# Optimization experiments

Hardware: AMD Instinct MI355X
Metric: run time of the kernel (lower is better)

Reference implementation:

```python
import jax, jax.numpy as jnp
import numpy as np

D = 1024
H = 4 * D
E = 8
K = 2


def setup_inputs() -> dict:
    key = jax.random.key(0)
    ks = jax.random.split(key, 8)
    s = 1.0 / np.sqrt(D)
    sh = 1.0 / np.sqrt(H)
    return {
        "x": jax.random.normal(ks[0], (4, 2048, D), dtype=jnp.float32),
        "gate_w": jax.random.uniform(ks[1], (D, E), jnp.float32, -s, s),
        "gate_b": jax.random.uniform(ks[2], (E,), jnp.float32, -s, s),
        "w1": jax.random.uniform(ks[3], (E, D, H), jnp.float32, -s, s),
        "b1": jax.random.uniform(ks[4], (E, H), jnp.float32, -s, s),
        "w2": jax.random.uniform(ks[5], (E, H, D), jnp.float32, -sh, sh),
        "b2": jax.random.uniform(ks[6], (E, D), jnp.float32, -sh, sh),
    }


def reference(x, gate_w, gate_b, w1, b1, w2, b2):
    # Gating: softmax over experts, top-k, renormalize.
    gate_logits = jnp.einsum("bsd,de->bse", x, gate_w) + gate_b
    weights = jax.nn.softmax(gate_logits, axis=-1)
    top_w, top_idx = jax.lax.top_k(weights, K)  # [B,S,K]
    top_w = top_w / jnp.sum(top_w, axis=-1, keepdims=True)

    out = jnp.zeros_like(x)
    # Loop over the fixed, small set of experts; dense FFN per expert,
    # masked-weighted combine (same math as the per-token torch loop).
    for e in range(E):
        # combine weight for expert e per token: sum of top_w where selected
        w_e = jnp.sum(jnp.where(top_idx == e, top_w, 0.0), axis=-1)  # [B,S]
        h = jax.nn.gelu(jnp.einsum("bsd,dh->bsh", x, w1[e]) + b1[e], approximate=False)
        y = jnp.einsum("bsh,hd->bsd", h, w2[e]) + b2[e]
        out = out + w_e[..., None] * y
    return out
```

## Files before the change

kernel.cpp:

```cpp
#include <hip/hip_runtime.h>
#include <math.h>

#define T_TOK 8192
#define DDIM  1024
#define HDIM  4096
#define NEXP  8
#define BM    128
#define BN    128
#define BK    64
#define MAXROWS (T_TOK*2 + NEXP*BM)
#define MAXTILES (MAXROWS/BM)
#define KS2   2
#define NGATE (T_TOK/8)
#define NTR1  ((HDIM/64)*(DDIM/64)*NEXP)
#define NTR2  ((DDIM/64)*(HDIM/64)*NEXP)

typedef __attribute__((ext_vector_type(8))) short short8;
typedef __attribute__((ext_vector_type(4))) short short4v;
typedef __attribute__((ext_vector_type(4))) float f32x4;

typedef const __attribute__((address_space(1))) unsigned int* gp1_t;
typedef __attribute__((address_space(3))) unsigned int* lp3_t;

__device__ __forceinline__ void gld16(const void* g, void* l) {
  __builtin_amdgcn_global_load_lds((gp1_t)g, (lp3_t)l, 16, 0, 0);
}

__device__ __forceinline__ short f2bf(float f) {
  unsigned u = __float_as_uint(f);
  u += 0x7fffu + ((u >> 16) & 1u);
  return (short)(u >> 16);
}

__device__ __forceinline__ float erf_fast(float x) {
  float ax = fabsf(x);
  float t = 1.f / (1.f + 0.3275911f * ax);
  float poly = t * (0.254829592f + t * (-0.284496736f + t * (1.421413741f +
               t * (-1.453152027f + t * 1.061405429f))));
  float r = 1.f - poly * __expf(-ax * ax);
  return copysignf(r, x);
}

__device__ __forceinline__ void tr_body(float* sl ,
    const float* __restrict__ w, short* __restrict__ wt, int R, int C, int lb) {
  int ctiles = C / 64, rtiles = R / 64;
  int e  = lb / (ctiles * rtiles);
  int rm = lb % (ctiles * rtiles);
  int r0 = (rm / ctiles) * 64;
  int c0 = (rm % ctiles) * 64;
  const float* W = w + (size_t)e * R * C;
  short* O = wt + (size_t)e * R * C;
  int t = threadIdx.x;
  int lr = t >> 4, lc4 = (t & 15) * 4;
#pragma unroll
  for (int i = 0; i < 4; i++) {
    float4 v = *(const float4*)&W[(size_t)(r0 + lr + i * 16) * C + c0 + lc4];
    sl[(lr + i * 16) * 65 + lc4 + 0] = v.x;
    sl[(lr + i * 16) * 65 + lc4 + 1] = v.y;
    sl[(lr + i * 16) * 65 + lc4 + 2] = v.z;
    sl[(lr + i * 16) * 65 + lc4 + 3] = v.w;
  }
  __syncthreads();
#pragma unroll
  for (int i = 0; i < 4; i++) {
    int oc = lr + i * 16;
    short4v s;
#pragma unroll
    for (int j = 0; j < 4; j++) s[j] = f2bf(sl[(lc4 + j) * 65 + oc]);
    *(short4v*)&O[(size_t)(c0 + oc) * R + r0 + lc4] = s;
  }
}

__device__ __forceinline__ void gate_body(char* smem, int bid,
    const float* __restrict__ x, const float* __restrict__ gw,
    const float* __restrict__ gb, int2* __restrict__ toke,
    float2* __restrict__ tokw, int* __restrict__ bcnt, short* __restrict__ xb) {
  float* sg = (float*)smem;
  int* lcnt = (int*)(smem + NEXP * DDIM * 4);
  int t = threadIdx.x;
#pragma unroll
  for (int it = 0; it < 8; ++it) {
    int l0 = (it * 256 + t) * 4;
    float4 v = *(const float4*)&gw[l0];
    int d = l0 >> 3, e0 = l0 & 7;
    sg[(e0 + 0) * DDIM + d] = v.x;
    sg[(e0 + 1) * DDIM + d] = v.y;
    sg[(e0 + 2) * DDIM + d] = v.z;
    sg[(e0 + 3) * DDIM + d] = v.w;
  }
  if (t < NEXP) lcnt[t] = 0;
  __syncthreads();
  int wave = t >> 6, lane = t & 63;
  int tok0 = bid * 8 + wave * 2;
#pragma unroll
  for (int tk = 0; tk < 2; ++tk) {
    int tok = tok0 + tk;
    float p[NEXP];
#pragma unroll
    for (int e = 0; e < NEXP; e++) p[e] = 0.f;
#pragma unroll
    for (int c = 0; c < 4; c++) {
      int d = c * 256 + lane * 4;
      float4 xv = *(const float4*)&x[(size_t)tok * DDIM + d];
      short4v sv;
      sv[0] = f2bf(xv.x); sv[1] = f2bf(xv.y); sv[2] = f2bf(xv.z); sv[3] = f2bf(xv.w);
      *(short4v*)&xb[(size_t)tok * DDIM + d] = sv;
#pragma unroll
      for (int e = 0; e < NEXP; e++) {
        float4 g = *(const float4*)&sg[e * DDIM + d];
        p[e] += xv.x * g.x + xv.y * g.y + xv.z * g.z + xv.w * g.w;
      }
    }
#pragma unroll
    for (int off = 32; off; off >>= 1)
#pragma unroll
      for (int e = 0; e < NEXP; e++) p[e] += __shfl_xor(p[e], off);
    if (lane == 0) {
      float l[NEXP];
#pragma unroll
      for (int e = 0; e < NEXP; e++) l[e] = p[e] + gb[e];
      int i0 = 0;
#pragma unroll
      for (int e = 1; e < NEXP; e++) if (l[e] > l[i0]) i0 = e;
      int i1 = (i0 == 0) ? 1 : 0;
#pragma unroll
      for (int e = 0; e < NEXP; e++) if (e != i0 && l[e] > l[i1]) i1 = e;
      float ex = expf(l[i1] - l[i0]);
      float w0 = 1.f / (1.f + ex);
      toke[tok] = make_int2(i0, i1);
      tokw[tok] = make_float2(w0, 1.f - w0);
      atomicAdd(&lcnt[i0], 1);
      atomicAdd(&lcnt[i1], 1);
    }
  }
  __syncthreads();
  if (t < NEXP) bcnt[bid * NEXP + t] = lcnt[t];
}

__global__ __launch_bounds__(256) void k_front(const float* __restrict__ x,
    const float* __restrict__ gw, const float* __restrict__ gb,
    const float* __restrict__ w1, const float* __restrict__ w2,
    int2* __restrict__ toke, float2* __restrict__ tokw, int* __restrict__ bcnt,
    short* __restrict__ xb, short* __restrict__ w1t, short* __restrict__ w2t) {
  __shared__ char smem[NEXP * DDIM * 4 + 64];
  int bid = blockIdx.x;
  if (bid < NGATE) {
    gate_body(smem, bid, x, gw, gb, toke, tokw, bcnt, xb);
  } else if (bid < NGATE + NTR1) {
    tr_body((float*)smem, w1, w1t, DDIM, HDIM, bid - NGATE);
  } else {
    tr_body((float*)smem, w2, w2t, HDIM, DDIM, bid - NGATE - NTR1);
  }
}

__global__ __launch_bounds__(256) void k_plan(const int* __restrict__ bcnt,
    int* __restrict__ pbase, int* __restrict__ texp) {
  __shared__ int tot[NEXP];
  __shared__ int b[NEXP + 1];
  int t = threadIdx.x;
  if (t < NEXP) tot[t] = 0;
  __syncthreads();
  int e = t & 7, sum = 0;
  for (int i = t >> 3; i < NGATE; i += 32) sum += bcnt[i * NEXP + e];
  atomicAdd(&tot[e], sum);
  __syncthreads();
  if (t == 0) {
    b[0] = 0;
#pragma unroll
    for (int ee = 0; ee < NEXP; ee++)
      b[ee + 1] = b[ee] + ((tot[ee] + BM - 1) & ~(BM - 1));
#pragma unroll
    for (int ee = 0; ee < NEXP; ee++) pbase[ee] = b[ee];
  }
  __syncthreads();
  for (int i = t; i < MAXTILES; i += 256) {
    int r0 = i * BM, ee = -1;
#pragma unroll
    for (int k = 0; k < NEXP; k++) if (r0 >= b[k] && r0 < b[k + 1]) ee = k;
    texp[i] = ee;
  }
}

__global__ __launch_bounds__(256) void k_scatter(const int2* __restrict__ toke,
    const float2* __restrict__ tokw, const int* __restrict__ pbase,
    int* __restrict__ fill, int* __restrict__ rtok, float* __restrict__ rwgt,
    int* __restrict__ trow) {
  int tok = blockIdx.x * 256 + threadIdx.x;
  if (tok >= T_TOK) return;
  int2 te = toke[tok];
  float2 tw = tokw[tok];
  int s0 = atomicAdd(&fill[te.x], 1);
  int r0 = pbase[te.x] + s0;
  rtok[r0] = tok; rwgt[r0] = tw.x; trow[tok * 2] = r0;
  int s1 = atomicAdd(&fill[te.y], 1);
  int r1 = pbase[te.y] + s1;
  rtok[r1] = tok; rwgt[r1] = tw.y; trow[tok * 2 + 1] = r1;
}

__global__ __launch_bounds__(256) void k_out(const float* __restrict__ out2,
    const float* __restrict__ b2, const int2* __restrict__ toke,
    const float2* __restrict__ tokw, const int* __restrict__ trow,
    float* __restrict__ out) {
  int idx = blockIdx.x * 256 + threadIdx.x;
  int tok = idx >> 8;
  int seg = (idx & 255) * 4;
  int2 te = toke[tok];
  float2 tw = tokw[tok];
  int r0 = trow[tok * 2], r1 = trow[tok * 2 + 1];
  float4 a  = *(const float4*)&out2[(size_t)r0 * DDIM + seg];
  float4 c  = *(const float4*)&out2[(size_t)r1 * DDIM + seg];
  float4 p0 = *(const float4*)&b2[te.x * DDIM + seg];
  float4 p1 = *(const float4*)&b2[te.y * DDIM + seg];
  float4 o;
  o.x = tw.x * (a.x + p0.x) + tw.y * (c.x + p1.x);
  o.y = tw.x * (a.y + p0.y) + tw.y * (c.y + p1.y);
  o.z = tw.x * (a.z + p0.z) + tw.y * (c.z + p1.z);
  o.w = tw.x * (a.w + p0.w) + tw.y * (c.w + p1.w);
  *(float4*)&out[(size_t)tok * DDIM + seg] = o;
}


#define STG(ko) { \
  gld16(sA[0] + (ko), &AL[(0 * 32 + wid * 8) * BK]); \
  gld16(sA[1] + (ko), &AL[(1 * 32 + wid * 8) * BK]); \
  gld16(sA[2] + (ko), &AL[(2 * 32 + wid * 8) * BK]); \
  gld16(sA[3] + (ko), &AL[(3 * 32 + wid * 8) * BK]); \
  gld16(sB[0] + (ko), &BL[(0 * 32 + wid * 8) * BK]); \
  gld16(sB[1] + (ko), &BL[(1 * 32 + wid * 8) * BK]); \
  gld16(sB[2] + (ko), &BL[(2 * 32 + wid * 8) * BK]); \
  gld16(sB[3] + (ko), &BL[(3 * 32 + wid * 8) * BK]); }

#define MFMA_TILE { \
  __builtin_amdgcn_s_setprio(1); \
  _Pragma("unroll") \
  for (int s = 0; s < 2; ++s) { \
    int xo = ((s * 4 + kg) ^ x7) << 3; \
    short8 af[4], bg[4]; \
    _Pragma("unroll") \
    for (int i = 0; i < 4; i++) af[i] = *(short8*)&AL[(wm + i * 16 + lr) * BK + xo]; \
    _Pragma("unroll") \
    for (int j = 0; j < 4; j++) bg[j] = *(short8*)&BL[(wn + j * 16 + lr) * BK + xo]; \
    _Pragma("unroll") \
    for (int i = 0; i < 4; i++) \
    _Pragma("unroll") \
    for (int j = 0; j < 4; j++) \
      acc[i][j] = __builtin_amdgcn_mfma_f32_16x16x32_bf16(af[i], bg[j], acc[i][j], 0, 0, 0); \
  } \
  __builtin_amdgcn_s_setprio(0); }

#define GEMM_LOOP(NKv) \
  for (int kt = 0; kt < (NKv); ++kt) { \
    STG(kt * BK); \
    asm volatile("s_waitcnt vmcnt(0)" ::: "memory"); \
    __syncthreads(); \
    MFMA_TILE; \
    __syncthreads(); \
  }

__global__ __launch_bounds__(256, 4) void k_ffn1(const short* __restrict__ xb,
    const short* __restrict__ w1t, const float* __restrict__ b1,
    const int* __restrict__ rtok, const int* __restrict__ texp,
    int tile_base, short* __restrict__ hbuf) {
  int tl = blockIdx.y;
  int tm = tile_base + tl;
  int e = texp[tm];
  if (e < 0) return;
  int n0 = blockIdx.x * BN;
  const short* W = w1t + (size_t)e * HDIM * DDIM;
  __shared__ short LDSBUF[2 * BM * BK];
  short* AL = LDSBUF;
  short* BL = LDSBUF + BM * BK;
  int t = threadIdx.x, wid = t >> 6, lane = t & 63;
  int sr8 = lane >> 3, slot = lane & 7;
  int swz = (slot ^ sr8) * 8;
  const short* sA[4]; const short* sB[4];
#pragma unroll
  for (int i = 0; i < 4; i++) {
    int r = i * 32 + wid * 8 + sr8;
    int tok = rtok[tm * BM + r]; if (tok < 0) tok = 0;
    sA[i] = xb + (size_t)tok * DDIM + swz;
    sB[i] = W + (size_t)(n0 + r) * DDIM + swz;
  }

  f32x4 acc[4][4];
#pragma unroll
  for (int i = 0; i < 4; i++)
#pragma unroll
    for (int j = 0; j < 4; j++) acc[i][j] = (f32x4){0.f, 0.f, 0.f, 0.f};

  int wm = (wid >> 1) * 64, wn = (wid & 1) * 64;
  int lr = lane & 15, kg = lane >> 4, x7 = lr & 7;

  GEMM_LOOP(DDIM / BK)

  short* SB = LDSBUF + wid * (32 * 68);
#pragma unroll
  for (int p = 0; p < 2; ++p) {
#pragma unroll
    for (int i2 = 0; i2 < 2; ++i2) {
      int i = p * 2 + i2;
#pragma unroll
      for (int j = 0; j < 4; ++j) {
        int col = j * 16 + lr;
        float bias = b1[e * HDIM + n0 + wn + col];
#pragma unroll
        for (int r = 0; r < 4; ++r) {
          float v = acc[i][j][r] + bias;
          v = 0.5f * v * (1.f + erf_fast(v * 0.70710678118f));
          SB[(i2 * 16 + kg * 4 + r) * 68 + col] = f2bf(v);
        }
      }
    }
    int lrow = lane >> 1, c0 = (lane & 1) * 32;
    size_t grow = (size_t)(tl * BM + wm + p * 32 + lrow);
#pragma unroll
    for (int s = 0; s < 4; ++s) {
      short8 v = *(short8*)&SB[lrow * 68 + c0 + s * 8];
      *(short8*)&hbuf[grow * HDIM + n0 + wn + c0 + s * 8] = v;
    }
  }
}

__global__ __launch_bounds__(256, 4) void k_ffn2d(const short* __restrict__ hbuf,
    const short* __restrict__ w2t, const int* __restrict__ texp,
    int tile_base, float* __restrict__ out2) {
  int tm = tile_base + blockIdx.y;
  int e = texp[tm];
  if (e < 0) return;
  int n0 = blockIdx.x * BN;
  const short* W = w2t + (size_t)e * DDIM * HDIM;
  __shared__ short LDSBUF[2 * BM * BK];
  short* AL = LDSBUF;
  short* BL = LDSBUF + BM * BK;
  int t = threadIdx.x, wid = t >> 6, lane = t & 63;
  int sr8 = lane >> 3, slot = lane & 7;
  int swz = (slot ^ sr8) * 8;
  const short* sA[4]; const short* sB[4];
#pragma unroll
  for (int i = 0; i < 4; i++) {
    int r = i * 32 + wid * 8 + sr8;
    sA[i] = hbuf + (size_t)(tm * BM + r) * HDIM + swz;
    sB[i] = W + (size_t)(n0 + r) * HDIM + swz;
  }

  f32x4 acc[4][4];
#pragma unroll
  for (int i = 0; i < 4; i++)
#pragma unroll
    for (int j = 0; j < 4; j++) acc[i][j] = (f32x4){0.f, 0.f, 0.f, 0.f};

  int wm = (wid >> 1) * 64, wn = (wid & 1) * 64;
  int lr = lane & 15, kg = lane >> 4, x7 = lr & 7;

  GEMM_LOOP(HDIM / BK)

  float* SBf = (float*)LDSBUF + wid * (16 * 68);
#pragma unroll
  for (int i = 0; i < 4; ++i) {
#pragma unroll
    for (int j = 0; j < 4; ++j)
#pragma unroll
      for (int r = 0; r < 4; ++r)
        SBf[(kg * 4 + r) * 68 + j * 16 + lr] = acc[i][j][r];
    int lrow = lane >> 2, c0 = (lane & 3) * 16;
    size_t grow = (size_t)(tm * BM + wm + i * 16 + lrow);
#pragma unroll
    for (int s = 0; s < 4; ++s) {
      float4 v = *(float4*)&SBf[lrow * 68 + c0 + s * 4];
      *(float4*)&out2[grow * DDIM + n0 + wn + c0 + s * 4] = v;
    }
  }
}

__global__ __launch_bounds__(256, 4) void k_ffn2a(const short* __restrict__ hbuf,
    const short* __restrict__ w2t, const float* __restrict__ b2,
    const int* __restrict__ rtok, const float* __restrict__ rwgt,
    const int* __restrict__ texp, int tile_base, float* __restrict__ out) {
  int tl = blockIdx.z;
  int tm = tile_base + tl;
  int e = texp[tm];
  if (e < 0) return;
  int kc = blockIdx.y;
  int n0 = blockIdx.x * BN;
  const short* W = w2t + (size_t)e * DDIM * HDIM;
  __shared__ short LDSBUF[2 * BM * BK];
  short* AL = LDSBUF;
  short* BL = LDSBUF + BM * BK;
  int t = threadIdx.x, wid = t >> 6, lane = t & 63;
  int sr8 = lane >> 3, slot = lane & 7;
  int swz = (slot ^ sr8) * 8;
  const int NK = HDIM / BK / KS2;
  int kbase = kc * NK * BK;
  const short* sA[4]; const short* sB[4];
#pragma unroll
  for (int i = 0; i < 4; i++) {
    int r = i * 32 + wid * 8 + sr8;
    sA[i] = hbuf + (size_t)(tl * BM + r) * HDIM + kbase + swz;
    sB[i] = W + (size_t)(n0 + r) * HDIM + kbase + swz;
  }
  f32x4 acc[4][4];
#pragma unroll
  for (int i = 0; i < 4; i++)
#pragma unroll
    for (int j = 0; j < 4; j++) acc[i][j] = (f32x4){0.f, 0.f, 0.f, 0.f};
  int wm = (wid >> 1) * 64, wn = (wid & 1) * 64;
  int lr = lane & 15, kg = lane >> 4, x7 = lr & 7;

  GEMM_LOOP(NK)

#pragma unroll
  for (int j = 0; j < 4; j++) {
    int gcol = n0 + wn + j * 16 + lr;
    float bias = (kc == 0) ? b2[e * DDIM + gcol] : 0.f;
#pragma unroll
    for (int i = 0; i < 4; i++) {
      int rl = wm + i * 16 + kg * 4;
#pragma unroll
      for (int r = 0; r < 4; r++) {
        int grow = tm * BM + rl + r;
        int tok = rtok[grow];
        if (tok >= 0) {
          float v = (acc[i][j][r] + bias) * rwgt[grow];
          atomicAdd(&out[(size_t)tok * DDIM + gcol], v);
        }
      }
    }
  }
}

extern "C" void kernel_launch(void* const* d_in, const int* in_sizes, int n_in,
                              void* d_out, int out_size, void* d_ws, size_t ws_size,
                              hipStream_t stream) {
  const float* x  = (const float*)d_in[0];
  const float* gw = (const float*)d_in[1];
  const float* gb = (const float*)d_in[2];
  const float* w1 = (const float*)d_in[3];
  const float* b1 = (const float*)d_in[4];
  const float* w2 = (const float*)d_in[5];
  const float* b2 = (const float*)d_in[6];
  float* out = (float*)d_out;
  char* ws = (char*)d_ws;

  int*    fill  = (int*)(ws + 32);
  int*    pbase = (int*)(ws + 64);
  int*    texp  = (int*)(ws + 128);
  int*    rtok  = (int*)(ws + 1024);
  float*  rwgt  = (float*)(ws + 1024 + (size_t)MAXROWS * 4);
  int2*   toke  = (int2*)(ws + 1024 + (size_t)MAXROWS * 8);
  float2* tokw  = (float2*)(ws + 1024 + (size_t)MAXROWS * 8 + (size_t)T_TOK * 8);
  int*    bcnt  = (int*)(ws + 640 * 1024);
  int*    trow  = (int*)(ws + 768 * 1024);
  size_t wbytes = (size_t)NEXP * DDIM * HDIM * 2;
  short*  w1t   = (short*)(ws + (1 << 20));
  short*  w2t   = (short*)(ws + (1 << 20) + wbytes);
  short*  xb    = (short*)(ws + (1 << 20) + 2 * wbytes);
  size_t xend   = (1 << 20) + 2 * wbytes + (size_t)T_TOK * DDIM * 2;
  size_t o2b    = (size_t)MAXROWS * DDIM * 4;
  size_t hbytes = (size_t)MAXTILES * BM * HDIM * 2;

  bool dense = ws_size >= xend + o2b + hbytes;

  hipMemsetAsync(ws, 0, 128, stream);
  hipMemsetAsync(rtok, 0xFF, (size_t)MAXROWS * 4, stream);

  k_front<<<NGATE + NTR1 + NTR2, 256, 0, stream>>>(x, gw, gb, w1, w2,
                                                   toke, tokw, bcnt, xb, w1t, w2t);
  k_plan<<<1, 256, 0, stream>>>(bcnt, pbase, texp);
  k_scatter<<<T_TOK / 256, 256, 0, stream>>>(toke, tokw, pbase, fill, rtok, rwgt, trow);

  if (dense) {
    float* out2 = (float*)(ws + xend);
    short* hbuf = (short*)(ws + xend + o2b);
    k_ffn1<<<dim3(HDIM / BN, MAXTILES), 256, 0, stream>>>(xb, w1t, b1, rtok, texp,
                                                          0, hbuf);
    const int HALF = MAXTILES / 2;
    k_ffn2d<<<dim3(DDIM / BN, HALF), 256, 0, stream>>>(hbuf, w2t, texp, 0, out2);
    k_ffn2d<<<dim3(DDIM / BN, MAXTILES - HALF), 256, 0, stream>>>(hbuf, w2t, texp,
                                                                  HALF, out2);
    k_out<<<(T_TOK * DDIM / 4) / 256, 256, 0, stream>>>(out2, b2, toke, tokw, trow, out);
  } else {
    short* hbuf = (short*)(ws + xend);
    size_t hcap = ws_size > xend ? ws_size - xend : 0;
    int tpc = (int)(hcap / ((size_t)BM * HDIM * 2));
    if (tpc < 1) return;
    if (tpc > MAXTILES) tpc = MAXTILES;
    hipMemsetAsync(d_out, 0, (size_t)T_TOK * DDIM * 4, stream);
    for (int base = 0; base < MAXTILES; base += tpc) {
      int nt = MAXTILES - base;
      if (nt > tpc) nt = tpc;
      k_ffn1<<<dim3(HDIM / BN, nt), 256, 0, stream>>>(xb, w1t, b1, rtok, texp, base, hbuf);
      k_ffn2a<<<dim3(DDIM / BN, KS2, nt), 256, 0, stream>>>(hbuf, w2t, b2, rtok, rwgt,
                                                            texp, base, out);
    }
  }
}
```

Baseline: 607.7 us.

## Store FFN2 partials as bf16, cheaper erf, unroll GEMM loop, single ffn2 launch

The second-FFN per-row outputs are now written as bf16 instead of fp32, which halves the intermediate buffer and the traffic into the combine kernel. The erf approximation is swapped for a lower-order rational form that uses a hardware reciprocal and no exp. The GEMM k-loop gets an unroll-4 pragma, and the two half-size ffn2 launches are merged into one. The cost is lower accuracy in the GELU and in the pre-combine expert outputs.

New measurement: 558.5 us. 1.09x faster.

```diff
diff --git a/kernel.cpp b/kernel.cpp
--- a/kernel.cpp
+++ b/kernel.cpp
@@ -32,12 +32,15 @@
   return (short)(u >> 16);
 }
 
+__device__ __forceinline__ float bf2f(short s) {
+  return __uint_as_float(((unsigned)(unsigned short)s) << 16);
+}
+
 __device__ __forceinline__ float erf_fast(float x) {
   float ax = fabsf(x);
-  float t = 1.f / (1.f + 0.3275911f * ax);
-  float poly = t * (0.254829592f + t * (-0.284496736f + t * (1.421413741f +
-               t * (-1.453152027f + t * 1.061405429f))));
-  float r = 1.f - poly * __expf(-ax * ax);
+  float t = 1.f + ax * (0.278393f + ax * (0.230389f + ax * (0.000972f + ax * 0.078108f)));
+  float t2 = t * t;
+  float r = 1.f - __builtin_amdgcn_rcpf(t2 * t2);
   return copysignf(r, x);
 }
 
@@ -197,7 +200,7 @@
   rtok[r1] = tok; rwgt[r1] = tw.y; trow[tok * 2 + 1] = r1;
 }
 
-__global__ __launch_bounds__(256) void k_out(const float* __restrict__ out2,
+__global__ __launch_bounds__(256) void k_out(const short* __restrict__ out2b,
     const float* __restrict__ b2, const int2* __restrict__ toke,
     const float2* __restrict__ tokw, const int* __restrict__ trow,
     float* __restrict__ out) {
@@ -207,15 +210,15 @@
   int2 te = toke[tok];
   float2 tw = tokw[tok];
   int r0 = trow[tok * 2], r1 = trow[tok * 2 + 1];
-  float4 a  = *(const float4*)&out2[(size_t)r0 * DDIM + seg];
-  float4 c  = *(const float4*)&out2[(size_t)r1 * DDIM + seg];
+  short4v a4 = *(const short4v*)&out2b[(size_t)r0 * DDIM + seg];
+  short4v c4 = *(const short4v*)&out2b[(size_t)r1 * DDIM + seg];
   float4 p0 = *(const float4*)&b2[te.x * DDIM + seg];
   float4 p1 = *(const float4*)&b2[te.y * DDIM + seg];
   float4 o;
-  o.x = tw.x * (a.x + p0.x) + tw.y * (c.x + p1.x);
-  o.y = tw.x * (a.y + p0.y) + tw.y * (c.y + p1.y);
-  o.z = tw.x * (a.z + p0.z) + tw.y * (c.z + p1.z);
-  o.w = tw.x * (a.w + p0.w) + tw.y * (c.w + p1.w);
+  o.x = tw.x * (bf2f(a4[0]) + p0.x) + tw.y * (bf2f(c4[0]) + p1.x);
+  o.y = tw.x * (bf2f(a4[1]) + p0.y) + tw.y * (bf2f(c4[1]) + p1.y);
+  o.z = tw.x * (bf2f(a4[2]) + p0.z) + tw.y * (bf2f(c4[2]) + p1.z);
+  o.w = tw.x * (bf2f(a4[3]) + p0.w) + tw.y * (bf2f(c4[3]) + p1.w);
   *(float4*)&out[(size_t)tok * DDIM + seg] = o;
 }
 
@@ -249,6 +252,7 @@
   __builtin_amdgcn_s_setprio(0); }
 
 #define GEMM_LOOP(NKv) \
+  _Pragma("unroll 4") \
   for (int kt = 0; kt < (NKv); ++kt) { \
     STG(kt * BK); \
     asm volatile("s_waitcnt vmcnt(0)" ::: "memory"); \
@@ -323,7 +327,7 @@
 
 __global__ __launch_bounds__(256, 4) void k_ffn2d(const short* __restrict__ hbuf,
     const short* __restrict__ w2t, const int* __restrict__ texp,
-    int tile_base, float* __restrict__ out2) {
+    int tile_base, short* __restrict__ out2b) {
   int tm = tile_base + blockIdx.y;
   int e = texp[tm];
   if (e < 0) return;
@@ -354,20 +358,20 @@
 
   GEMM_LOOP(HDIM / BK)
 
-  float* SBf = (float*)LDSBUF + wid * (16 * 68);
+  short* SB = LDSBUF + wid * (16 * 68);
 #pragma unroll
   for (int i = 0; i < 4; ++i) {
 #pragma unroll
     for (int j = 0; j < 4; ++j)
 #pragma unroll
       for (int r = 0; r < 4; ++r)
-        SBf[(kg * 4 + r) * 68 + j * 16 + lr] = acc[i][j][r];
+        SB[(kg * 4 + r) * 68 + j * 16 + lr] = f2bf(acc[i][j][r]);
     int lrow = lane >> 2, c0 = (lane & 3) * 16;
     size_t grow = (size_t)(tm * BM + wm + i * 16 + lrow);
 #pragma unroll
-    for (int s = 0; s < 4; ++s) {
-      float4 v = *(float4*)&SBf[lrow * 68 + c0 + s * 4];
-      *(float4*)&out2[grow * DDIM + n0 + wn + c0 + s * 4] = v;
+    for (int s = 0; s < 2; ++s) {
+      short8 v = *(short8*)&SB[lrow * 68 + c0 + s * 8];
+      *(short8*)&out2b[grow * DDIM + n0 + wn + c0 + s * 8] = v;
     }
   }
 }
@@ -455,7 +459,7 @@
   short*  w2t   = (short*)(ws + (1 << 20) + wbytes);
   short*  xb    = (short*)(ws + (1 << 20) + 2 * wbytes);
   size_t xend   = (1 << 20) + 2 * wbytes + (size_t)T_TOK * DDIM * 2;
-  size_t o2b    = (size_t)MAXROWS * DDIM * 4;
+  size_t o2b    = (size_t)MAXROWS * DDIM * 2;
   size_t hbytes = (size_t)MAXTILES * BM * HDIM * 2;
 
   bool dense = ws_size >= xend + o2b + hbytes;
@@ -469,15 +473,12 @@
   k_scatter<<<T_TOK / 256, 256, 0, stream>>>(toke, tokw, pbase, fill, rtok, rwgt, trow);
 
   if (dense) {
-    float* out2 = (float*)(ws + xend);
-    short* hbuf = (short*)(ws + xend + o2b);
+    short* out2b = (short*)(ws + xend);
+    short* hbuf  = (short*)(ws + xend + o2b);
     k_ffn1<<<dim3(HDIM / BN, MAXTILES), 256, 0, stream>>>(xb, w1t, b1, rtok, texp,
                                                           0, hbuf);
-    const int HALF = MAXTILES / 2;
-    k_ffn2d<<<dim3(DDIM / BN, HALF), 256, 0, stream>>>(hbuf, w2t, texp, 0, out2);
-    k_ffn2d<<<dim3(DDIM / BN, MAXTILES - HALF), 256, 0, stream>>>(hbuf, w2t, texp,
-                                                                  HALF, out2);
-    k_out<<<(T_TOK * DDIM / 4) / 256, 256, 0, stream>>>(out2, b2, toke, tokw, trow, out);
+    k_ffn2d<<<dim3(DDIM / BN, MAXTILES), 256, 0, stream>>>(hbuf, w2t, texp, 0, out2b);
+    k_out<<<(T_TOK * DDIM / 4) / 256, 256, 0, stream>>>(out2b, b2, toke, tokw, trow, out);
   } else {
     short* hbuf = (short*)(ws + xend);
     size_t hcap = ws_size > xend ? ws_size - xend : 0;
```
